# Kernel tuning notes

Measured on AMD Instinct MI355X. Metric: run time of the kernel, lower is better.

## Reference

```python
import jax, jax.numpy as jnp
import numpy as np

BERT_DIM, HIDDEN, LABELS, UFD = 768, 256, 9, 20
B, R, S = 64, 16, 64


def _masked_mean(x, mask, axis):
    # x: [..., axis, d], mask: [..., axis] float 0/1 -> masked mean over `axis`
    num = jnp.sum(x * mask[..., None], axis=axis)
    den = jnp.maximum(jnp.sum(mask, axis=axis), 1e-9)[..., None]
    return num / den


def setup_inputs() -> dict:
    key = jax.random.key(0)
    ks = jax.random.split(key, 8)
    sc = 0.02
    return {
        "inputs": jax.random.normal(ks[0], (B, R, S, BERT_DIM), jnp.float32),
        "user_feats": jax.random.normal(ks[1], (B, UFD), jnp.float32),
        "W_proj": jax.random.normal(ks[2], (BERT_DIM, HIDDEN), jnp.float32) * sc,
        "b_proj": jnp.zeros((HIDDEN,), jnp.float32),
        "W_rff": jax.random.normal(ks[3], (HIDDEN + UFD, 1), jnp.float32) * sc,
        "b_rff": jnp.zeros((1,), jnp.float32),
        "W_pff": jax.random.normal(ks[4], (HIDDEN + UFD, LABELS), jnp.float32) * sc,
        "b_pff": jnp.zeros((LABELS,), jnp.float32),
        "user_w": jnp.ones((UFD,), jnp.float32),
    }


def reference(inputs, user_feats, W_proj, b_proj, W_rff, b_rff, W_pff, b_pff, user_w):
    # projection: [B,R,S,bert] -> [B,R,S,H]
    x = jnp.einsum("brsd,dh->brsh", inputs, W_proj) + b_proj
    # sentence-level DAN: mask = sum over hidden != 0 (as in source, post-projection)
    s_mask = (jnp.sum(x, axis=-1) != 0).astype(x.dtype)          # [B,R,S]
    r_hn = _masked_mean(x, s_mask, axis=2)                        # [B,R,H]
    # review-level DAN
    r_mask = (jnp.sum(x, axis=(-1, -2)) != 0).astype(x.dtype)    # [B,R]
    p_hn = _masked_mean(r_hn, r_mask, axis=1)                     # [B,H]
    # F.normalize(user_feats) (L2 over dim=1, eps=1e-12) scaled by learned weights
    nrm = jnp.maximum(jnp.linalg.norm(user_feats, axis=1, keepdims=True), 1e-12)
    uf = (user_feats / nrm) * user_w
    p_batch = jnp.concatenate([p_hn, uf], axis=-1)                # [B,H+UFD]
    # review feedforward (Linear -> SELU), squeezed -> [B]
    r_stars = jax.nn.selu(p_batch @ W_rff + b_rff)[:, 0]
    # product DAN over the batch axis (no mask -> plain mean), then Linear+SELU
    h_n = jnp.mean(p_batch, axis=0)                               # [H+UFD]
    p_stars = jax.nn.selu(h_n @ W_pff + b_pff)                    # [LABELS]
    return p_stars, r_stars
```

## Files before the change

kernel.cpp:

```cpp
#include <hip/hip_runtime.h>
#include <cmath>

static constexpr int BERT   = 768;
static constexpr int HID    = 256;
static constexpr int NLAB   = 9;
static constexpr int NUFD   = 20;
static constexpr int NB     = 64;
static constexpr int NR     = 16;
static constexpr int NS     = 64;
static constexpr int PBD    = HID + NUFD;

typedef float v4f __attribute__((ext_vector_type(4)));

static constexpr size_t WS_A      = 0;
static constexpr size_t WS_COLSUM = 786432;
static constexpr size_t WS_SUMB   = 787200;
static constexpr size_t WS_CNT    = 787264;
static constexpr size_t WS_TSUM   = 788288;
static constexpr size_t WS_PB     = 789312;

__device__ __forceinline__ float selu_f(float x) {
    const float alpha = 1.6732632423543772848170429916717f;
    const float scale = 1.0507009873554804934193349852946f;
    return scale * (x > 0.0f ? x : alpha * (expf(x) - 1.0f));
}

__global__ __launch_bounds__(256) void k0_colsum(
    const float* __restrict__ W, const float* __restrict__ bp,
    float* __restrict__ colsum, float* __restrict__ sumb) {
    int blk = blockIdx.x;
    int tid = threadIdx.x;
    if (blk < 96) {
        int row    = blk * 8 + (tid >> 5);
        int lane32 = tid & 31;
        const v4f* W4 = (const v4f*)(W + (size_t)row * HID);
        v4f s4 = W4[lane32 * 2] + W4[lane32 * 2 + 1];
        float s = (s4.x + s4.y) + (s4.z + s4.w);
        #pragma unroll
        for (int off = 16; off > 0; off >>= 1) s += __shfl_xor(s, off);
        if (lane32 == 0) colsum[row] = s;
    } else {
        __shared__ float red[256];
        red[tid] = bp[tid];
        __syncthreads();
        for (int s = 128; s > 0; s >>= 1) {
            if (tid < s) red[tid] += red[tid + s];
            __syncthreads();
        }
        if (tid == 0) *sumb = red[0];
    }
}

__global__ __launch_bounds__(256) void k1_reduce(
    const float* __restrict__ inp, const float* __restrict__ colsum,
    const float* __restrict__ sumb, float* __restrict__ A,
    float* __restrict__ cnt_g, float* __restrict__ tsum_g) {
    int br  = blockIdx.x;
    int tid = threadIdx.x;
    int w = tid >> 6, l = tid & 63;

    const v4f* cs4 = (const v4f*)colsum;
    v4f c0 = cs4[l], c1 = cs4[64 + l], c2 = cs4[128 + l];
    float sb = *sumb;

    const v4f* base = (const v4f*)(inp + (size_t)br * NS * BERT);
    v4f a0 = {0.f,0.f,0.f,0.f};
    v4f a1 = {0.f,0.f,0.f,0.f};
    v4f a2 = {0.f,0.f,0.f,0.f};
    float p[16];

    #pragma unroll 4
    for (int i = 0; i < 16; ++i) {
        int s = w * 16 + i;
        const v4f* rp = base + (size_t)s * (BERT / 4);
        v4f v0 = __builtin_nontemporal_load(rp + l);
        v4f v1 = __builtin_nontemporal_load(rp + 64 + l);
        v4f v2 = __builtin_nontemporal_load(rp + 128 + l);
        p[i] = v0.x*c0.x + v0.y*c0.y + v0.z*c0.z + v0.w*c0.w
             + v1.x*c1.x + v1.y*c1.y + v1.z*c1.z + v1.w*c1.w
             + v2.x*c2.x + v2.y*c2.y + v2.z*c2.z + v2.w*c2.w;
        a0 += v0; a1 += v1; a2 += v2;
    }

    #pragma unroll
    for (int off = 32; off > 0; off >>= 1) {
        #pragma unroll
        for (int i = 0; i < 16; ++i) p[i] += __shfl_xor(p[i], off);
    }

    float cnt = 0.f, ts = 0.f;
    bool anyzero = false;
    #pragma unroll
    for (int i = 0; i < 16; ++i) {
        float t = p[i] + sb;
        ts += t;
        cnt += (t != 0.0f) ? 1.0f : 0.0f;
        anyzero |= (t == 0.0f);
    }
    if (anyzero) {
        for (int i = 0; i < 16; ++i) {
            if (p[i] + sb == 0.0f) {
                int s = w * 16 + i;
                const v4f* rp = base + (size_t)s * (BERT / 4);
                a0 -= rp[l]; a1 -= rp[64 + l]; a2 -= rp[128 + l];
            }
        }
    }

    __shared__ float part[4][BERT];
    __shared__ float cw[4], tw[4];
    float* pw = part[w];
    ((v4f*)pw)[l]       = a0;
    ((v4f*)pw)[64 + l]  = a1;
    ((v4f*)pw)[128 + l] = a2;
    if (l == 0) { cw[w] = cnt; tw[w] = ts; }
    __syncthreads();

    float* Ao = A + (size_t)br * BERT;
    for (int c = tid; c < BERT; c += 256)
        Ao[c] = (part[0][c] + part[1][c]) + (part[2][c] + part[3][c]);
    if (tid == 0) {
        cnt_g[br]  = (cw[0] + cw[1]) + (cw[2] + cw[3]);
        tsum_g[br] = (tw[0] + tw[1]) + (tw[2] + tw[3]);
    }
}

__global__ __launch_bounds__(256) void k2_gemm(
    const float* __restrict__ A, const float* __restrict__ cnt_g,
    const float* __restrict__ tsum_g, const float* __restrict__ W_proj,
    const float* __restrict__ b_proj, const float* __restrict__ user_feats,
    const float* __restrict__ user_w, float* __restrict__ pb_out) {
    int b   = blockIdx.x >> 2;
    int q   = blockIdx.x & 3;
    int tid = threadIdx.x;

    __shared__ float M[BERT];
    __shared__ float g[NR];
    __shared__ float scal[2];
    __shared__ float red[256];

    if (tid < NR) {
        float c  = cnt_g[b * NR + tid];
        float t  = tsum_g[b * NR + tid];
        float rm = (t != 0.0f) ? 1.0f : 0.0f;
        float den = fmaxf(c, 1e-9f);
        g[tid]        = rm / den;
        red[tid]      = rm;
        red[NR + tid] = rm * (c / den);
    }
    __syncthreads();
    if (tid == 0) {
        float srm = 0.f, sq = 0.f;
        for (int r = 0; r < NR; ++r) { srm += red[r]; sq += red[NR + r]; }
        scal[0] = fmaxf(srm, 1e-9f);
        scal[1] = sq;
    }
    for (int c = tid; c < BERT; c += 256) {
        float m = 0.f;
        #pragma unroll
        for (int r = 0; r < NR; ++r)
            m += g[r] * A[(size_t)(b * NR + r) * BERT + c];
        M[c] = m;
    }
    __syncthreads();

    int hl = tid & 63;
    int ks = tid >> 6;
    int h  = q * 64 + hl;
    {
        const float* Wc = W_proj + h;
        float acc = 0.f;
        int d0 = ks * 192;
        #pragma unroll 16
        for (int j = 0; j < 192; ++j)
            acc += M[d0 + j] * Wc[(size_t)(d0 + j) * HID];
        red[tid] = acc;
    }
    __syncthreads();
    if (tid < 64) {
        float s = (red[tid] + red[64 + tid]) + (red[128 + tid] + red[192 + tid]);
        int hh = q * 64 + tid;
        pb_out[b * PBD + hh] = (s + b_proj[hh] * scal[1]) / scal[0];
    }

    if (q == 0) {
        __syncthreads();
        if (tid == 0) {
            float s = 0.f;
            for (int j = 0; j < NUFD; ++j) {
                float v = user_feats[b * NUFD + j];
                s += v * v;
            }
            red[0] = 1.0f / fmaxf(sqrtf(s), 1e-12f);
        }
        __syncthreads();
        if (tid < NUFD)
            pb_out[b * PBD + HID + tid] =
                user_feats[b * NUFD + tid] * red[0] * user_w[tid];
    }
}

__global__ __launch_bounds__(320) void k3_final(
    const float* __restrict__ pb, const float* __restrict__ W_rff,
    const float* __restrict__ b_rff, const float* __restrict__ W_pff,
    const float* __restrict__ b_pff, float* __restrict__ out) {
    __shared__ float hn[PBD];
    int tid = threadIdx.x;
    if (tid < PBD) {
        float s = 0.f;
        #pragma unroll 8
        for (int b = 0; b < NB; ++b) s += pb[b * PBD + tid];
        hn[tid] = s * (1.0f / NB);
    }
    __syncthreads();
    if (tid < NB) {
        int b = tid;
        float acc = 0.f;
        #pragma unroll 12
        for (int j = 0; j < PBD; ++j) acc += pb[b * PBD + j] * W_rff[j];
        out[NLAB + b] = selu_f(acc + b_rff[0]);
    } else if (tid >= 64 && tid < 64 + NLAB) {
        int lab = tid - 64;
        float acc = 0.f;
        #pragma unroll 12
        for (int j = 0; j < PBD; ++j) acc += hn[j] * W_pff[j * NLAB + lab];
        out[lab] = selu_f(acc + b_pff[lab]);
    }
}

extern "C" void kernel_launch(void* const* d_in, const int* in_sizes, int n_in,
                              void* d_out, int out_size, void* d_ws, size_t ws_size,
                              hipStream_t stream) {
    const float* inputs     = (const float*)d_in[0];
    const float* user_feats = (const float*)d_in[1];
    const float* W_proj     = (const float*)d_in[2];
    const float* b_proj     = (const float*)d_in[3];
    const float* W_rff      = (const float*)d_in[4];
    const float* b_rff      = (const float*)d_in[5];
    const float* W_pff      = (const float*)d_in[6];
    const float* b_pff      = (const float*)d_in[7];
    const float* user_w     = (const float*)d_in[8];
    float* out = (float*)d_out;
    float* ws  = (float*)d_ws;

    float* A      = ws + WS_A;
    float* colsum = ws + WS_COLSUM;
    float* sumb   = ws + WS_SUMB;
    float* cntg   = ws + WS_CNT;
    float* tsumg  = ws + WS_TSUM;
    float* pb     = ws + WS_PB;

    hipLaunchKernelGGL(k0_colsum, dim3(97), dim3(256), 0, stream,
                       W_proj, b_proj, colsum, sumb);
    hipLaunchKernelGGL(k1_reduce, dim3(NB * NR), dim3(256), 0, stream,
                       inputs, colsum, sumb, A, cntg, tsumg);
    hipLaunchKernelGGL(k2_gemm, dim3(NB * 4), dim3(256), 0, stream,
                       A, cntg, tsumg, W_proj, b_proj, user_feats, user_w, pb);
    hipLaunchKernelGGL(k3_final, dim3(1), dim3(320), 0, stream,
                       pb, W_rff, b_rff, W_pff, b_pff, out);
}
```

Before: 299.2 us.

## Split per-review reduction across four blocks with atomic accumulation

Each review's 64-sentence reduction is now split across four blocks of 16 sentences instead of one block of 64, quadrupling the grid so the streaming of the large input tensor has more parallelism and latency hiding. Partial sums are combined with float atomicAdd into the A, count and tsum buffers, which the first kernel now zeroes with extra blocks. Nontemporal loads are dropped in favour of plain loads. This adds atomic traffic, a zeroing pass, and order-dependent float summation.

```diff
diff --git a/kernel.cpp b/kernel.cpp
--- a/kernel.cpp
+++ b/kernel.cpp
@@ -27,7 +27,9 @@
 
 __global__ __launch_bounds__(256) void k0_colsum(
     const float* __restrict__ W, const float* __restrict__ bp,
-    float* __restrict__ colsum, float* __restrict__ sumb) {
+    float* __restrict__ colsum, float* __restrict__ sumb,
+    float* __restrict__ A, float* __restrict__ cnt_g,
+    float* __restrict__ tsum_g) {
     int blk = blockIdx.x;
     int tid = threadIdx.x;
     if (blk < 96) {
@@ -39,7 +41,7 @@
         #pragma unroll
         for (int off = 16; off > 0; off >>= 1) s += __shfl_xor(s, off);
         if (lane32 == 0) colsum[row] = s;
-    } else {
+    } else if (blk == 96) {
         __shared__ float red[256];
         red[tid] = bp[tid];
         __syncthreads();
@@ -48,6 +50,17 @@
             __syncthreads();
         }
         if (tid == 0) *sumb = red[0];
+    } else if (blk == 97) {
+        #pragma unroll
+        for (int i = 0; i < 4; ++i) {
+            cnt_g[i * 256 + tid]  = 0.0f;
+            tsum_g[i * 256 + tid] = 0.0f;
+        }
+    } else {
+        const int nz = 1024 - 98;
+        for (size_t idx = (size_t)(blk - 98) * 256 + tid;
+             idx < (size_t)1024 * BERT; idx += (size_t)nz * 256)
+            A[idx] = 0.0f;
     }
 }
 
@@ -55,7 +68,9 @@
     const float* __restrict__ inp, const float* __restrict__ colsum,
     const float* __restrict__ sumb, float* __restrict__ A,
     float* __restrict__ cnt_g, float* __restrict__ tsum_g) {
-    int br  = blockIdx.x;
+    int g   = blockIdx.x;
+    int br  = g >> 2;
+    int q4  = g & 3;
     int tid = threadIdx.x;
     int w = tid >> 6, l = tid & 63;
 
@@ -64,18 +79,19 @@
     float sb = *sumb;
 
     const v4f* base = (const v4f*)(inp + (size_t)br * NS * BERT);
+    int s0 = q4 * 16 + w * 4;
+
     v4f a0 = {0.f,0.f,0.f,0.f};
     v4f a1 = {0.f,0.f,0.f,0.f};
     v4f a2 = {0.f,0.f,0.f,0.f};
-    float p[16];
-
-    #pragma unroll 4
-    for (int i = 0; i < 16; ++i) {
-        int s = w * 16 + i;
-        const v4f* rp = base + (size_t)s * (BERT / 4);
-        v4f v0 = __builtin_nontemporal_load(rp + l);
-        v4f v1 = __builtin_nontemporal_load(rp + 64 + l);
-        v4f v2 = __builtin_nontemporal_load(rp + 128 + l);
+    float p[4];
+
+    #pragma unroll
+    for (int i = 0; i < 4; ++i) {
+        const v4f* rp = base + (size_t)(s0 + i) * (BERT / 4);
+        v4f v0 = rp[l];
+        v4f v1 = rp[64 + l];
+        v4f v2 = rp[128 + l];
         p[i] = v0.x*c0.x + v0.y*c0.y + v0.z*c0.z + v0.w*c0.w
              + v1.x*c1.x + v1.y*c1.y + v1.z*c1.z + v1.w*c1.w
              + v2.x*c2.x + v2.y*c2.y + v2.z*c2.z + v2.w*c2.w;
@@ -85,23 +101,22 @@
     #pragma unroll
     for (int off = 32; off > 0; off >>= 1) {
         #pragma unroll
-        for (int i = 0; i < 16; ++i) p[i] += __shfl_xor(p[i], off);
+        for (int i = 0; i < 4; ++i) p[i] += __shfl_xor(p[i], off);
     }
 
     float cnt = 0.f, ts = 0.f;
     bool anyzero = false;
     #pragma unroll
-    for (int i = 0; i < 16; ++i) {
+    for (int i = 0; i < 4; ++i) {
         float t = p[i] + sb;
         ts += t;
         cnt += (t != 0.0f) ? 1.0f : 0.0f;
         anyzero |= (t == 0.0f);
     }
     if (anyzero) {
-        for (int i = 0; i < 16; ++i) {
+        for (int i = 0; i < 4; ++i) {
             if (p[i] + sb == 0.0f) {
-                int s = w * 16 + i;
-                const v4f* rp = base + (size_t)s * (BERT / 4);
+                const v4f* rp = base + (size_t)(s0 + i) * (BERT / 4);
                 a0 -= rp[l]; a1 -= rp[64 + l]; a2 -= rp[128 + l];
             }
         }
@@ -118,10 +133,10 @@
 
     float* Ao = A + (size_t)br * BERT;
     for (int c = tid; c < BERT; c += 256)
-        Ao[c] = (part[0][c] + part[1][c]) + (part[2][c] + part[3][c]);
+        atomicAdd(&Ao[c], (part[0][c] + part[1][c]) + (part[2][c] + part[3][c]));
     if (tid == 0) {
-        cnt_g[br]  = (cw[0] + cw[1]) + (cw[2] + cw[3]);
-        tsum_g[br] = (tw[0] + tw[1]) + (tw[2] + tw[3]);
+        atomicAdd(&cnt_g[br],  (cw[0] + cw[1]) + (cw[2] + cw[3]));
+        atomicAdd(&tsum_g[br], (tw[0] + tw[1]) + (tw[2] + tw[3]));
     }
 }
 
@@ -250,9 +265,9 @@
     float* tsumg  = ws + WS_TSUM;
     float* pb     = ws + WS_PB;
 
-    hipLaunchKernelGGL(k0_colsum, dim3(97), dim3(256), 0, stream,
-                       W_proj, b_proj, colsum, sumb);
-    hipLaunchKernelGGL(k1_reduce, dim3(NB * NR), dim3(256), 0, stream,
+    hipLaunchKernelGGL(k0_colsum, dim3(1024), dim3(256), 0, stream,
+                       W_proj, b_proj, colsum, sumb, A, cntg, tsumg);
+    hipLaunchKernelGGL(k1_reduce, dim3(NB * NR * 4), dim3(256), 0, stream,
                        inputs, colsum, sumb, A, cntg, tsumg);
     hipLaunchKernelGGL(k2_gemm, dim3(NB * 4), dim3(256), 0, stream,
                        A, cntg, tsumg, W_proj, b_proj, user_feats, user_w, pb);
```

After: 313.4 us. 4.7% more time.
